# Kernel tuning notes

Measured on AMD Instinct MI355X. Metric: run time of the kernel, lower is better.

Reference implementation:

```python
import jax, jax.numpy as jnp
import numpy as np

PI = 3.141592653589793


def conv2d(x, w, b=None, padding=0, groups=1):
    out = jax.lax.conv_general_dilated(
        x, w, window_strides=(1, 1), padding=((padding, padding), (padding, padding)),
        dimension_numbers=('NCHW', 'OIHW', 'NCHW'), feature_group_count=groups)
    if b is not None:
        out = out + b.reshape(1, -1, 1, 1)
    return out


def group_norm(x, weight, bias, num_groups, eps=1e-5):
    B, C, H, W = x.shape
    xg = x.reshape(B, num_groups, C // num_groups, H, W)
    mean = xg.mean(axis=(2, 3, 4), keepdims=True)
    var = xg.var(axis=(2, 3, 4), keepdims=True)
    xg = (xg - mean) / jnp.sqrt(var + eps)
    return xg.reshape(B, C, H, W) * weight.reshape(1, -1, 1, 1) + bias.reshape(1, -1, 1, 1)


def l2norm(x, eps=1e-12):
    n = jnp.sqrt(jnp.sum(x * x, axis=1, keepdims=True))
    return x / jnp.maximum(n, eps)


def dense_sift(x):
    # kornia DenseSIFTDescriptor defaults: 8 angle bins, 4x4 spatial bins, bin size 4,
    # stride 1, padding 1, rootsift=True, clipval=0.2. Input (B,1,H,W) -> (B,128,H,W).
    eps = 1e-10
    B, C, H, W = x.shape
    # spatial_gradient(x, 'diff'), normalized: central differences / 2, replicate pad
    p = jnp.pad(x, ((0, 0), (0, 0), (1, 1), (1, 1)), mode='edge')
    gx = (p[:, :, 1:-1, 2:] - p[:, :, 1:-1, :-2]) * 0.5
    gy = (p[:, :, 2:, 1:-1] - p[:, :, :-2, 1:-1]) * 0.5
    mag = jnp.sqrt(gx * gx + gy * gy + eps)
    ori = jnp.arctan2(gy, gx + eps) + 2.0 * PI
    o_big = 8.0 * ori / (2.0 * PI)
    bo0f = jnp.floor(o_big)
    wo1 = o_big - bo0f
    bo0 = bo0f % 8
    bo1 = (bo0 + 1) % 8
    wo0m = (1.0 - wo1) * mag
    wo1m = wo1 * mag
    bins = jnp.arange(8, dtype=x.dtype).reshape(1, 8, 1, 1)
    # soft orientation-histogram binning -> (B,8,H,W)
    ang = jnp.where(bo0 == bins, wo0m, 0.0) + jnp.where(bo1 == bins, wo1m, 0.0)
    # triangular bin pooling kernel (ksize=4), depthwise conv, pad 2 -> (B,8,H+1,W+1)
    ks2 = 2.0
    xc2 = ks2 - jnp.abs(jnp.arange(4, dtype=x.dtype) + 0.5 - ks2)
    pk = jnp.outer(xc2, xc2) / (ks2 ** 2)
    pk = jnp.tile(pk.reshape(1, 1, 4, 4), (8, 1, 1, 1))
    pooled = jax.lax.conv_general_dilated(
        ang, pk, (1, 1), ((2, 2), (2, 2)),
        dimension_numbers=('NCHW', 'OIHW', 'NCHW'), feature_group_count=8)
    # PoolingConv with identity reshape kernel (k=4, pad=1) == 4x4 patch extraction
    pp = jnp.pad(pooled, ((0, 0), (0, 0), (1, 1), (1, 1)))
    patches = jnp.stack([pp[:, :, y:y + H, xx:xx + W]
                         for y in range(4) for xx in range(4)], axis=2)  # (B,8,16,H,W)
    out = patches.reshape(B, 128, H, W)
    out = jnp.clip(l2norm(out), 0.0, 0.2)
    out = l2norm(out)
    # rootsift: sqrt(L1-normalized + eps)
    l1 = jnp.sum(jnp.abs(out), axis=1, keepdims=True)
    out = jnp.sqrt(out / jnp.maximum(l1, 1e-12) + eps)
    return out


def gauss1d(ks, sigma):
    t = jnp.arange(ks, dtype=jnp.float32) - (ks - 1) / 2.0
    g = jnp.exp(-(t * t) / (2.0 * sigma * sigma))
    return g / g.sum()


def joint_bilateral_blur(inp, guidance, ks=5, sigma_color=0.1, sigma_space=(1.5, 1.5)):
    # kornia joint_bilateral_blur: border_type='reflect', color_distance_type='l1'
    B, C, H, W = inp.shape
    pad = ks // 2
    pi_ = jnp.pad(inp, ((0, 0), (0, 0), (pad, pad), (pad, pad)), mode='reflect')
    pg = jnp.pad(guidance, ((0, 0), (0, 0), (pad, pad), (pad, pad)), mode='reflect')

    def unfold(p):  # (B,C,H,W,ks*ks), flatten order (dy, dx)
        return jnp.stack([p[:, :, y:y + H, x:x + W]
                          for y in range(ks) for x in range(ks)], axis=-1)

    ui = unfold(pi_)
    ug = unfold(pg)
    diff = ug - guidance[..., None]
    cdist_sq = jnp.square(jnp.sum(jnp.abs(diff), axis=1, keepdims=True))  # L1 over channels, squared
    color_k = jnp.exp(-0.5 / (sigma_color ** 2) * cdist_sq)               # (B,1,H,W,K2)
    space_k = jnp.outer(gauss1d(ks, sigma_space[0]), gauss1d(ks, sigma_space[1])).reshape(1, 1, 1, 1, -1)
    kernel = space_k * color_k
    return (ui * kernel).sum(-1) / kernel.sum(-1)


def setup_inputs() -> dict:
    key = jax.random.key(0)
    ks = jax.random.split(key, 8)
    B, H, W = 4, 270, 512

    def wgt(k, shape, scale=0.05):
        return jax.random.normal(k, shape, dtype=jnp.float32) * scale

    z = lambda n: jnp.zeros((n,), dtype=jnp.float32)
    o = lambda n: jnp.ones((n,), dtype=jnp.float32)
    return {
        'x': jax.random.normal(ks[0], (B, 1, H, W), dtype=jnp.float32),
        'w1': wgt(ks[1], (64, 128, 5, 5)), 'b1': z(64), 'g1w': o(64), 'g1b': z(64),
        'w2': wgt(ks[2], (32, 64, 3, 3)), 'b2': z(32), 'g2w': o(32), 'g2b': z(32),
        'w3': wgt(ks[3], (16, 32, 3, 3)), 'b3': z(16), 'g3w': o(16), 'g3b': z(16),
        'w4': wgt(ks[4], (8, 16, 3, 3)), 'b4': z(8), 'g4w': o(8), 'g4b': z(8),
        'w5': wgt(ks[5], (2, 8, 3, 3)), 'b5': z(2),
        'sw1': wgt(ks[6], (32, 128, 1, 1)), 'sb1': z(32),
        'sw2': wgt(ks[7], (8, 32, 1, 1)), 'sb2': z(8),
    }


def reference(x, w1, b1, g1w, g1b, w2, b2, g2w, g2b, w3, b3, g3w, g3b,
              w4, b4, g4w, g4b, w5, b5, sw1, sb1, sw2, sb2):
    orig = x
    s = dense_sift(x)                                     # (B,128,H,W)
    h = jax.nn.relu(group_norm(conv2d(s, w1, b1, 2), g1w, g1b, 8))
    h = jax.nn.relu(group_norm(conv2d(h, w2, b2, 1), g2w, g2b, 8))
    h = h + conv2d(s, sw1, sb1, 0)                        # skip 1
    blk = h
    h = jax.nn.relu(group_norm(conv2d(h, w3, b3, 1), g3w, g3b, 4))
    h = jax.nn.relu(group_norm(conv2d(h, w4, b4, 1), g4w, g4b, 4))
    h = h + conv2d(blk, sw2, sb2, 0)                      # skip 2
    h = conv2d(h, w5, b5, 1)                              # (B,2,H,W)
    guide = jnp.tile(orig, (1, 2, 1, 1))
    h = joint_bilateral_blur(h, guide, ks=5, sigma_color=0.1, sigma_space=(1.5, 1.5))
    h = jnp.tanh(h)
    scale = jnp.array([0.436, 0.615], dtype=h.dtype).reshape(1, 2, 1, 1)
    return h * scale
```

## Files before the change

### kernel.cpp

```cpp
#include <hip/hip_runtime.h>

#define DEV __device__ __forceinline__

typedef __bf16 bf16x8 __attribute__((ext_vector_type(8)));
typedef float f32x4 __attribute__((ext_vector_type(4)));

union U8 { uint4 q; unsigned short u[8]; };

constexpr int BN = 4, H = 270, W = 512, HW = H * W;
constexpr int IH5 = 274, P5 = 516;
constexpr int IH3 = 272, P3 = 514;

DEV unsigned short f2bf(float f) {
  unsigned int u = __builtin_bit_cast(unsigned int, f);
  u = (u + 0x7FFFu + ((u >> 16) & 1u)) >> 16;
  return (unsigned short)u;
}
DEV float bf2f(unsigned short h) {
  return __builtin_bit_cast(float, (unsigned int)h << 16);
}

#define GLL16(g, l)                                                                        \
  __builtin_amdgcn_global_load_lds((const __attribute__((address_space(1))) void*)(g),     \
                                   (__attribute__((address_space(3))) void*)(l), 16, 0, 0)

DEV int swz(int row) { return ((row >> 1) & 3) << 4; }

__global__ void k_fill(float* __restrict__ out, int n, float v) {
  int i = blockIdx.x * 256 + threadIdx.x;
  if (i < n) out[i] = v;
}

template <int C, int PD>
__global__ void k_halo(unsigned short* __restrict__ buf, int IHt, int pitch, int nb_) {
  int vPerRow = pitch * C / 8;
  int topBot = 2 * PD * vPerRow;
  int sideV = PD * C / 8;
  int midRows = IHt - 2 * PD;
  int perS = topBot + midRows * 2 * sideV;
  int v = blockIdx.x * 256 + threadIdx.x;
  if (v >= nb_ * perS) return;
  int s = v / perS, r = v % perS;
  size_t base = (size_t)s * IHt * pitch * C;
  size_t off;
  if (r < topBot) {
    int half = r / (PD * vPerRow);
    int rr = r % (PD * vPerRow);
    off = ((size_t)(half ? (IHt - PD) : 0) * pitch * C) + (size_t)rr * 8;
  } else {
    int r2 = r - topBot;
    int row = r2 / (2 * sideV), c2 = r2 % (2 * sideV);
    int side = c2 / sideV, cc = c2 % sideV;
    off = ((size_t)(PD + row) * pitch + (side ? (pitch - PD) : 0)) * C + (size_t)cc * 8;
  }
  *(uint4*)(buf + base + off) = uint4{0, 0, 0, 0};
}

__global__ void k_sift_ang(const float* __restrict__ x, float* __restrict__ ang, int nTot) {
  int p = blockIdx.x * 256 + threadIdx.x;
  if (p >= nTot) return;
  int b = p / HW, r = p % HW, y = r / W, xx = r % W;
  const float* xb = x + (size_t)b * HW;
  float xm = xb[y * W + (xx > 0 ? xx - 1 : 0)];
  float xp = xb[y * W + (xx < W - 1 ? xx + 1 : W - 1)];
  float ym = xb[(y > 0 ? y - 1 : 0) * W + xx];
  float yp = xb[(y < H - 1 ? y + 1 : H - 1) * W + xx];
  float gx = (xp - xm) * 0.5f, gy = (yp - ym) * 0.5f;
  float mag = sqrtf(gx * gx + gy * gy + 1e-10f);
  float ori = atan2f(gy, gx + 1e-10f) + 6.2831855f;
  float o = (8.0f * ori) / 6.2831855f;
  float bo0f = floorf(o);
  float wo1 = o - bo0f;
  int b0 = ((int)bo0f) & 7;
  int b1 = (b0 + 1) & 7;
  float w0m = (1.0f - wo1) * mag, w1m = wo1 * mag;
  float v[8];
#pragma unroll
  for (int k = 0; k < 8; ++k)
    v[k] = (k == b0 ? w0m : 0.0f) + (k == b1 ? w1m : 0.0f);
  float4* o4 = (float4*)(ang + (size_t)p * 8);
  o4[0] = make_float4(v[0], v[1], v[2], v[3]);
  o4[1] = make_float4(v[4], v[5], v[6], v[7]);
}

__global__ void k_sift_pool(const float* __restrict__ ang, float* __restrict__ pooled, int nTot) {
  constexpr int PH = H + 1, PW = W + 1;
  int p = blockIdx.x * 256 + threadIdx.x;
  if (p >= nTot) return;
  int b = p / (PH * PW), r = p % (PH * PW), y = r / PW, xx = r % PW;
  float4 a0 = {0, 0, 0, 0}, a1 = {0, 0, 0, 0};
  const float xc2[4] = {0.5f, 1.5f, 1.5f, 0.5f};
#pragma unroll
  for (int ky = 0; ky < 4; ++ky) {
    int yy = y - 2 + ky;
    if (yy < 0 || yy >= H) continue;
#pragma unroll
    for (int kx = 0; kx < 4; ++kx) {
      int xs = xx - 2 + kx;
      if (xs < 0 || xs >= W) continue;
      float w = xc2[ky] * xc2[kx] * 0.25f;
      const float4* s4 = (const float4*)(ang + ((size_t)(b * H + yy) * W + xs) * 8);
      float4 v0 = s4[0], v1 = s4[1];
      a0.x += w * v0.x; a0.y += w * v0.y; a0.z += w * v0.z; a0.w += w * v0.w;
      a1.x += w * v1.x; a1.y += w * v1.y; a1.z += w * v1.z; a1.w += w * v1.w;
    }
  }
  float4* o4 = (float4*)(pooled + (size_t)p * 8);
  o4[0] = a0; o4[1] = a1;
}

__global__ void k_sift_desc(const float* __restrict__ pooled, unsigned short* __restrict__ spad) {
  constexpr int PH = H + 1, PW = W + 1;
  int tid = threadIdx.x;
  int wv = tid >> 6, lane = tid & 63;
  int p = blockIdx.x * 4 + wv;
  int b = p / HW, r = p % HW, yy = r / W, xx = r % W;
  int a = lane >> 3, jj = lane & 7;
  int j0 = jj * 2;
  int dy = j0 >> 2, dx = j0 & 3;
  int rr = yy + dy - 1;
  int c0 = xx + dx - 1, c1 = c0 + 1;
  bool rv = (rr >= 0 && rr <= H);
  int rc = min(max(rr, 0), H);
  const float* pb = pooled + ((size_t)(b * PH + rc) * PW) * 8 + a;
  float v0 = 0.0f, v1 = 0.0f;
  if (rv && c0 >= 0 && c0 <= W) v0 = pb[(size_t)c0 * 8];
  if (rv && c1 >= 0 && c1 <= W) v1 = pb[(size_t)c1 * 8];

  float n2 = v0 * v0 + v1 * v1;
#pragma unroll
  for (int m = 1; m < 64; m <<= 1) n2 += __shfl_xor(n2, m);
  float inv = 1.0f / fmaxf(sqrtf(n2), 1e-12f);
  v0 = fminf(v0 * inv, 0.2f);
  v1 = fminf(v1 * inv, 0.2f);
  float S = v0 + v1;
#pragma unroll
  for (int m = 1; m < 64; m <<= 1) S += __shfl_xor(S, m);
  float iS = 1.0f / fmaxf(S, 1e-12f);
  v0 = sqrtf(v0 * iS + 1e-10f);
  v1 = sqrtf(v1 * iS + 1e-10f);
  unsigned int pk = (unsigned int)f2bf(v0) | ((unsigned int)f2bf(v1) << 16);
  *(unsigned int*)(spad + ((size_t)(b * IH5 + yy + 2) * P5 + xx + 2) * 128 + lane * 2) = pk;
}

template <int CIN, int COUT, int KS>
__global__ void k_prep(const float* __restrict__ w, unsigned short* __restrict__ wbuf) {
  int i = blockIdx.x * 256 + threadIdx.x;
  if (i >= KS * KS * COUT * CIN) return;
  int t = i / (COUT * CIN), r2 = i % (COUT * CIN), co = r2 / CIN, e = r2 % CIN;
  wbuf[i] = f2bf(w[(co * CIN + e) * (KS * KS) + t]);
}

DEV int xcd_remap(int bid, int nbid) {
  int q8 = nbid >> 3, r8 = nbid & 7;
  int xcd = bid & 7;
  return (xcd < r8 ? xcd * (q8 + 1) : r8 * (q8 + 1) + (xcd - r8) * q8) + (bid >> 3);
}

template <int CIN, int COUT, int KS, int NG, int MINW, bool FSKIP, int BMPX>
__launch_bounds__(BMPX, MINW)
__global__ void k_convr(const unsigned short* __restrict__ in, int IHt, int ipitch,
                        const unsigned short* __restrict__ wtap,
                        const float* __restrict__ bias,
                        const unsigned short* __restrict__ wsk,
                        const float* __restrict__ skb,
                        unsigned short* __restrict__ outraw,
                        unsigned short* __restrict__ skraw,
                        float* __restrict__ part, int nbid) {
  constexpr int NWV = BMPX / 64;
  constexpr int NXB = 512 / BMPX;
  constexpr int SLABPX = BMPX + KS - 1;
  constexpr int KQ = CIN / 32;
  constexpr int NF = COUT / 16;
  constexpr int SLAB = SLABPX * 64;
  constexpr int SWQ = COUT * 64;
  constexpr int SWROW = KS * SWQ;
  constexpr int SSK = FSKIP ? 32 * 64 : 16;
  constexpr int STRIDE = BMPX * 16;
  __shared__ __align__(16) unsigned char slabB[2][SLAB];
  __shared__ __align__(16) unsigned char wrowB[2][SWROW];
  __shared__ __align__(16) unsigned char wskB[2][SSK];
  __shared__ float red[NWV][16];

  int tid = threadIdx.x;
  int lane = tid & 63, wid = tid >> 6;
  int l15 = lane & 15, hi = lane >> 4;

  int byl = xcd_remap(blockIdx.x, nbid);
  int half = byl % NXB, rowid = byl / NXB;
  int y = rowid % H, b = rowid / H;
  int x0 = half * BMPX;

  f32x4 acc[4][NF] = {};
  f32x4 ask[4][2] = {};

  auto stage = [&](int it, int pbuf) {
    int q = it / KS, ky = it % KS;
    const char* src = (const char*)(in + ((size_t)(b * IHt + y + ky) * ipitch + x0) * CIN + q * 32);
    for (int d = tid * 16; d < SLAB; d += STRIDE) {
      int px = d >> 6, qb = d & 63;
      GLL16(src + px * (CIN * 2) + (qb ^ swz(px)), slabB[pbuf] + d);
    }
    const char* wsrc = (const char*)wtap + (size_t)(ky * KS) * (COUT * CIN * 2) + q * 64;
    for (int d = tid * 16; d < SWROW; d += STRIDE) {
      int kx = d / SWQ, rem = d % SWQ;
      int co = rem >> 6, qb = rem & 63;
      GLL16(wsrc + (size_t)kx * (COUT * CIN * 2) + co * (CIN * 2) + (qb ^ swz(co)), wrowB[pbuf] + d);
    }
  };
  auto stage_wsk = [&](int q, int pbuf) {
    const char* src = (const char*)wsk + q * 64;
    for (int d = tid * 16; d < 32 * 64; d += STRIDE) {
      int co = d >> 6, qb = d & 63;
      GLL16(src + co * (CIN * 2) + (qb ^ swz(co)), wskB[pbuf] + d);
    }
  };

  stage(0, 0);
  if constexpr (FSKIP) stage_wsk(0, 0);
  __syncthreads();

#pragma unroll 1
  for (int it = 0; it < KQ * KS; ++it) {
    int cur = it & 1;
    int q = it / KS, ky = it % KS;
    if (it + 1 < KQ * KS) {
      stage(it + 1, cur ^ 1);
      if (FSKIP && (it + 1) % KS == 0) stage_wsk((it + 1) / KS, ((it + 1) / KS) & 1);
    }
    const unsigned char* sl = slabB[cur];
    const unsigned char* wr = wrowB[cur];
    int koff = hi * 16;
#pragma unroll
    for (int kx = 0; kx < KS; ++kx) {
      bf16x8 af[4];
#pragma unroll
      for (int mi = 0; mi < 4; ++mi) {
        int px = wid * 64 + mi * 16 + l15 + kx;
        af[mi] = *(const bf16x8*)(sl + px * 64 + (koff ^ swz(px)));
      }
#pragma unroll
      for (int ni = 0; ni < NF; ++ni) {
        int co = ni * 16 + l15;
        bf16x8 bq = *(const bf16x8*)(wr + kx * SWQ + co * 64 + (koff ^ swz(co)));
#pragma unroll
        for (int mi = 0; mi < 4; ++mi)
          acc[mi][ni] = __builtin_amdgcn_mfma_f32_16x16x32_bf16(af[mi], bq, acc[mi][ni], 0, 0, 0);
      }
      if constexpr (FSKIP) {
        if (ky == KS / 2 && kx == KS / 2) {
#pragma unroll
          for (int ni = 0; ni < 2; ++ni) {
            int co = ni * 16 + l15;
            bf16x8 bq = *(const bf16x8*)(wskB[q & 1] + co * 64 + (koff ^ swz(co)));
#pragma unroll
            for (int mi = 0; mi < 4; ++mi)
              ask[mi][ni] = __builtin_amdgcn_mfma_f32_16x16x32_bf16(af[mi], bq, ask[mi][ni], 0, 0, 0);
          }
        }
      }
    }
    __syncthreads();
  }

#pragma unroll
  for (int ni = 0; ni < NF; ++ni) {
    float bv = bias[ni * 16 + l15];
#pragma unroll
    for (int mi = 0; mi < 4; ++mi)
#pragma unroll
      for (int rr = 0; rr < 4; ++rr)
        acc[mi][ni][rr] += bv;
  }
  unsigned short* op = outraw + ((size_t)(b * H + y) * W + x0) * COUT;
#pragma unroll
  for (int mi = 0; mi < 4; ++mi)
#pragma unroll
    for (int rr = 0; rr < 4; ++rr) {
      int px = wid * 64 + mi * 16 + hi * 4 + rr;
#pragma unroll
      for (int ni = 0; ni < NF; ++ni)
        op[(size_t)px * COUT + ni * 16 + l15] = f2bf(acc[mi][ni][rr]);
    }
  if constexpr (FSKIP) {
    unsigned short* ops = skraw + ((size_t)(b * H + y) * W + x0) * 32;
#pragma unroll
    for (int ni = 0; ni < 2; ++ni) {
      float bv = skb[ni * 16 + l15];
#pragma unroll
      for (int mi = 0; mi < 4; ++mi)
#pragma unroll
        for (int rr = 0; rr < 4; ++rr)
          ask[mi][ni][rr] += bv;
    }
#pragma unroll
    for (int mi = 0; mi < 4; ++mi)
#pragma unroll
      for (int rr = 0; rr < 4; ++rr) {
        int px = wid * 64 + mi * 16 + hi * 4 + rr;
#pragma unroll
        for (int ni = 0; ni < 2; ++ni)
          ops[(size_t)px * 32 + ni * 16 + l15] = f2bf(ask[mi][ni][rr]);
      }
  }
  if constexpr (NG > 0) {
    constexpr int GPC = COUT / NG;
#pragma unroll
    for (int ni = 0; ni < NF; ++ni) {
      float s = 0.0f, q2 = 0.0f;
#pragma unroll
      for (int mi = 0; mi < 4; ++mi)
#pragma unroll
        for (int rr = 0; rr < 4; ++rr) {
          float v = acc[mi][ni][rr];
          s += v; q2 += v * v;
        }
      s += __shfl_xor(s, 16); q2 += __shfl_xor(q2, 16);
      s += __shfl_xor(s, 32); q2 += __shfl_xor(q2, 32);
#pragma unroll
      for (int m = 1; m < GPC; m <<= 1) { s += __shfl_xor(s, m); q2 += __shfl_xor(q2, m); }
      if (hi == 0 && (l15 % GPC) == 0) {
        int g = ni * (16 / GPC) + l15 / GPC;
        red[wid][g] = s;
        red[wid][NG + g] = q2;
      }
    }
    __syncthreads();
    if (tid < 2 * NG) {
      float t = 0.0f;
#pragma unroll
      for (int wv2 = 0; wv2 < NWV; ++wv2) t += red[wv2][tid];
      part[(size_t)byl * (2 * NG) + tid] = t;
    }
  }
}

template <int CIN, int COUT, int KS, int NG, bool ADDSK>
__launch_bounds__(512, 4)
__global__ void k_convf(const unsigned short* __restrict__ in,
                        const unsigned short* __restrict__ skin,
                        const unsigned short* __restrict__ wtap,
                        const float* __restrict__ bias,
                        const float* __restrict__ scg, const float* __restrict__ shg,
                        unsigned short* __restrict__ outraw,
                        float* __restrict__ part, int nbid) {
  constexpr int SLABPX = 512 + KS - 1;
  constexpr int KQ = CIN / 32;
  constexpr int NF = COUT / 16;
  constexpr int SLAB = SLABPX * 64;
  constexpr int SWQ = COUT * 64;
  constexpr int SWROW = KS * SWQ;
  __shared__ __align__(16) unsigned char slabB[2][SLAB];
  __shared__ __align__(16) unsigned char wrowB[2][SWROW];
  __shared__ float scS[CIN], shS[CIN];
  __shared__ float red[8][16];

  int tid = threadIdx.x;
  int lane = tid & 63, wid = tid >> 6;
  int l15 = lane & 15, hi = lane >> 4;

  int byl = xcd_remap(blockIdx.x, nbid);
  int y = byl % H, b = byl / H;

  if (tid < CIN) { scS[tid] = scg[b * CIN + tid]; shS[tid] = shg[b * CIN + tid]; }
  __syncthreads();

  f32x4 acc[4][NF] = {};

  auto stage = [&](int it, int pbuf) {
    int q = it / KS, ky = it % KS;
    int row = y + ky - 1;
    bool rowok = (row >= 0 && row < H);
    for (int d = tid * 16; d < SLAB; d += 8192) {
      int px = d >> 6, qb = d & 63;
      int x = px - 1;
      U8 o; o.q = uint4{0, 0, 0, 0};
      if (rowok && x >= 0 && x < W) {
        size_t e = ((size_t)(b * H + row) * W + x) * CIN + q * 32;
        U8 u; u.q = *(const uint4*)((const char*)in + e * 2 + qb);
        U8 s;
        if (ADDSK) s.q = *(const uint4*)((const char*)skin + e * 2 + qb);
        int cb = q * 32 + (qb >> 1);
#pragma unroll
        for (int j = 0; j < 8; ++j) {
          float f = fmaxf(bf2f(u.u[j]) * scS[cb + j] + shS[cb + j], 0.0f);
          if (ADDSK) f += bf2f(s.u[j]);
          o.u[j] = f2bf(f);
        }
      }
      *(uint4*)(slabB[pbuf] + px * 64 + (qb ^ swz(px))) = o.q;
    }
    const char* wsrc = (const char*)wtap + (size_t)(ky * KS) * (COUT * CIN * 2) + q * 64;
    for (int d = tid * 16; d < SWROW; d += 8192) {
      int kx = d / SWQ, rem = d % SWQ;
      int co = rem >> 6, qb = rem & 63;
      GLL16(wsrc + (size_t)kx * (COUT * CIN * 2) + co * (CIN * 2) + (qb ^ swz(co)), wrowB[pbuf] + d);
    }
  };

  stage(0, 0);
  __syncthreads();

#pragma unroll 1
  for (int it = 0; it < KQ * KS; ++it) {
    int cur = it & 1;
    if (it + 1 < KQ * KS) stage(it + 1, cur ^ 1);
    const unsigned char* sl = slabB[cur];
    const unsigned char* wr = wrowB[cur];
    int koff = hi * 16;
#pragma unroll
    for (int kx = 0; kx < KS; ++kx) {
      bf16x8 af[4];
#pragma unroll
      for (int mi = 0; mi < 4; ++mi) {
        int px = wid * 64 + mi * 16 + l15 + kx;
        af[mi] = *(const bf16x8*)(sl + px * 64 + (koff ^ swz(px)));
      }
#pragma unroll
      for (int ni = 0; ni < NF; ++ni) {
        int co = ni * 16 + l15;
        bf16x8 bq = *(const bf16x8*)(wr + kx * SWQ + co * 64 + (koff ^ swz(co)));
#pragma unroll
        for (int mi = 0; mi < 4; ++mi)
          acc[mi][ni] = __builtin_amdgcn_mfma_f32_16x16x32_bf16(af[mi], bq, acc[mi][ni], 0, 0, 0);
      }
    }
    __syncthreads();
  }

#pragma unroll
  for (int ni = 0; ni < NF; ++ni) {
    float bv = bias[ni * 16 + l15];
#pragma unroll
    for (int mi = 0; mi < 4; ++mi)
#pragma unroll
      for (int rr = 0; rr < 4; ++rr)
        acc[mi][ni][rr] += bv;
  }
  unsigned short* op = outraw + ((size_t)(b * H + y) * W) * COUT;
#pragma unroll
  for (int mi = 0; mi < 4; ++mi)
#pragma unroll
    for (int rr = 0; rr < 4; ++rr) {
      int px = wid * 64 + mi * 16 + hi * 4 + rr;
#pragma unroll
      for (int ni = 0; ni < NF; ++ni)
        op[(size_t)px * COUT + ni * 16 + l15] = f2bf(acc[mi][ni][rr]);
    }
  if constexpr (NG > 0) {
    constexpr int GPC = COUT / NG;
#pragma unroll
    for (int ni = 0; ni < NF; ++ni) {
      float s = 0.0f, q2 = 0.0f;
#pragma unroll
      for (int mi = 0; mi < 4; ++mi)
#pragma unroll
        for (int rr = 0; rr < 4; ++rr) {
          float v = acc[mi][ni][rr];
          s += v; q2 += v * v;
        }
      s += __shfl_xor(s, 16); q2 += __shfl_xor(q2, 16);
      s += __shfl_xor(s, 32); q2 += __shfl_xor(q2, 32);
#pragma unroll
      for (int m = 1; m < GPC; m <<= 1) { s += __shfl_xor(s, m); q2 += __shfl_xor(q2, m); }
      if (hi == 0 && (l15 % GPC) == 0) {
        int g = ni * (16 / GPC) + l15 / GPC;
        red[wid][g] = s;
        red[wid][NG + g] = q2;
      }
    }
    __syncthreads();
    if (tid < 2 * NG) {
      float t = 0.0f;
#pragma unroll
      for (int wv2 = 0; wv2 < 8; ++wv2) t += red[wv2][tid];
      part[(size_t)byl * (2 * NG) + tid] = t;
    }
  }
}

template <int COUT, int NG>
__global__ void k_gn_fin(const float* __restrict__ part, int NB,
                         const float* __restrict__ gw, const float* __restrict__ gb,
                         float* __restrict__ scale, float* __restrict__ shift, float invN) {
  constexpr int GPC = COUT / NG;
  int b = blockIdx.x / NG, g = blockIdx.x % NG;
  int lane = threadIdx.x;
  float s = 0.0f, q = 0.0f;
  for (int i = lane; i < NB; i += 64) {
    const float* pp = part + (size_t)(b * NB + i) * (2 * NG);
    s += pp[g]; q += pp[NG + g];
  }
#pragma unroll
  for (int m = 1; m < 64; m <<= 1) { s += __shfl_xor(s, m); q += __shfl_xor(q, m); }
  if (lane == 0) {
    float mean = s * invN;
    float var = q * invN - mean * mean;
    float rstd = rsqrtf(var + 1e-5f);
#pragma unroll
    for (int j = 0; j < GPC; ++j) {
      int c = g * GPC + j;
      float sc = gw[c] * rstd;
      scale[b * COUT + c] = sc;
      shift[b * COUT + c] = gb[c] - mean * sc;
    }
  }
}

__global__ void k_conv4(const unsigned short* __restrict__ h3raw, const float* __restrict__ w4,
                        const float* __restrict__ b4,
                        const float* __restrict__ sc3, const float* __restrict__ sh3,
                        unsigned short* __restrict__ h4raw, float* __restrict__ part) {
  __shared__ float wl[1152];
  __shared__ float scs[16], shs[16];
  __shared__ float red[4][8];
  int b0 = (blockIdx.x * 256) / HW;
  for (int i = threadIdx.x; i < 1152; i += 256) {
    int t = i / 128, r2 = i % 128, ci = r2 >> 3, co = r2 & 7;
    wl[i] = w4[(co * 16 + ci) * 9 + t];
  }
  if (threadIdx.x < 16) { scs[threadIdx.x] = sc3[b0 * 16 + threadIdx.x]; shs[threadIdx.x] = sh3[b0 * 16 + threadIdx.x]; }
  __syncthreads();
  int p = blockIdx.x * 256 + threadIdx.x;
  int b = p / HW, r = p % HW, y = r / W, xx = r % W;
  float acc[8];
#pragma unroll
  for (int co = 0; co < 8; ++co) acc[co] = b4[co];
#pragma unroll
  for (int t = 0; t < 9; ++t) {
    int ky = t / 3, kx = t % 3;
    int row = y + ky - 1, x = xx + kx - 1;
    if (row < 0 || row >= H || x < 0 || x >= W) continue;
    const unsigned short* ip = h3raw + ((size_t)(b * H + row) * W + x) * 16;
    U8 u0, u1;
    u0.q = *(const uint4*)ip;
    u1.q = *(const uint4*)(ip + 8);
#pragma unroll
    for (int ci = 0; ci < 16; ++ci) {
      float raw = bf2f(ci < 8 ? u0.u[ci] : u1.u[ci - 8]);
      float iv = fmaxf(raw * scs[ci] + shs[ci], 0.0f);
#pragma unroll
      for (int co = 0; co < 8; ++co)
        acc[co] += iv * wl[t * 128 + ci * 8 + co];
    }
  }
  int lane = threadIdx.x & 63, wv = threadIdx.x >> 6;
  float s[4], q[4];
#pragma unroll
  for (int g = 0; g < 4; ++g) {
    s[g] = acc[2 * g] + acc[2 * g + 1];
    q[g] = acc[2 * g] * acc[2 * g] + acc[2 * g + 1] * acc[2 * g + 1];
  }
#pragma unroll
  for (int m = 1; m < 64; m <<= 1) {
#pragma unroll
    for (int g = 0; g < 4; ++g) { s[g] += __shfl_xor(s[g], m); q[g] += __shfl_xor(q[g], m); }
  }
  if (lane == 0) {
#pragma unroll
    for (int g = 0; g < 4; ++g) { red[wv][g] = s[g]; red[wv][4 + g] = q[g]; }
  }
  __syncthreads();
  if (threadIdx.x < 8)
    part[(size_t)blockIdx.x * 8 + threadIdx.x] =
        red[0][threadIdx.x] + red[1][threadIdx.x] + red[2][threadIdx.x] + red[3][threadIdx.x];
  U8 o;
#pragma unroll
  for (int co = 0; co < 8; ++co) o.u[co] = f2bf(acc[co]);
  *(uint4*)(h4raw + (size_t)p * 8) = o.q;
}

__global__ void k_norm4(const unsigned short* __restrict__ h4raw,
                        const unsigned short* __restrict__ h2raw,
                        const unsigned short* __restrict__ sk1,
                        const float* __restrict__ sc2, const float* __restrict__ sh2,
                        const float* __restrict__ sc4, const float* __restrict__ sh4,
                        const float* __restrict__ sw2, const float* __restrict__ sb2,
                        unsigned short* __restrict__ blk2pad) {
  __shared__ float wl[256];
  __shared__ float s2[32], h2s[32];
  int b0 = (blockIdx.x * 256) / HW;
  {
    int i = threadIdx.x;
    int ci = i >> 3, co = i & 7;
    wl[i] = sw2[co * 32 + ci];
    if (i < 32) { s2[i] = sc2[b0 * 32 + i]; h2s[i] = sh2[b0 * 32 + i]; }
  }
  __syncthreads();
  int p = blockIdx.x * 256 + threadIdx.x;
  int b = p / HW, r = p % HW, y = r / W, xx = r % W;
  float acc[8];
#pragma unroll
  for (int co = 0; co < 8; ++co) acc[co] = sb2[co];
  const unsigned short* hp2 = h2raw + (size_t)p * 32;
  const unsigned short* skp = sk1 + (size_t)p * 32;
#pragma unroll
  for (int half = 0; half < 4; ++half) {
    U8 u; u.q = *(const uint4*)(hp2 + half * 8);
    U8 s; s.q = *(const uint4*)(skp + half * 8);
#pragma unroll
    for (int j = 0; j < 8; ++j) {
      int ci = half * 8 + j;
      float blk = fmaxf(bf2f(u.u[j]) * s2[ci] + h2s[ci], 0.0f) + bf2f(s.u[j]);
#pragma unroll
      for (int co = 0; co < 8; ++co) acc[co] += blk * wl[ci * 8 + co];
    }
  }
  U8 hv; hv.q = *(const uint4*)(h4raw + (size_t)p * 8);
  U8 o;
#pragma unroll
  for (int co = 0; co < 8; ++co) {
    float f = fmaxf(bf2f(hv.u[co]) * sc4[b * 8 + co] + sh4[b * 8 + co], 0.0f) + acc[co];
    o.u[co] = f2bf(f);
  }
  size_t cbase = ((size_t)(b * IH3 + y + 1) * P3 + (xx + 1));
  *(uint4*)(blk2pad + cbase * 8) = o.q;
}

__global__ void k_conv5(const unsigned short* __restrict__ blk2pad, const float* __restrict__ w5,
                        const float* __restrict__ b5, float* __restrict__ h5) {
  __shared__ float wl[144];
  if (threadIdx.x < 144) {
    int i = threadIdx.x;
    int t = i / 16, r2 = i % 16, ci = r2 >> 1, co = r2 & 1;
    wl[i] = w5[(co * 8 + ci) * 9 + t];
  }
  __syncthreads();
  int p = blockIdx.x * 256 + threadIdx.x;
  int b = p / HW, r = p % HW, y = r / W, xx = r % W;
  float a0 = b5[0], a1 = b5[1];
#pragma unroll
  for (int t = 0; t < 9; ++t) {
    int ky = t / 3, kx = t % 3;
    const unsigned short* ip = blk2pad + ((size_t)(b * IH3 + y + ky) * P3 + (xx + kx)) * 8;
    U8 u; u.q = *(const uint4*)ip;
#pragma unroll
    for (int ci = 0; ci < 8; ++ci) {
      float iv = bf2f(u.u[ci]);
      a0 += iv * wl[t * 16 + ci * 2];
      a1 += iv * wl[t * 16 + ci * 2 + 1];
    }
  }
  h5[(size_t)p * 2] = a0;
  h5[(size_t)p * 2 + 1] = a1;
}

__global__ void k_bilateral(const float* __restrict__ h5, const float* __restrict__ x,
                            float* __restrict__ out, int nTot) {
  int p = blockIdx.x * 256 + threadIdx.x;
  if (p >= nTot) return;
  int b = p / HW, r = p % HW, y = r / W, xx = r % W;
  const float* xb = x + (size_t)b * HW;
  float xc = xb[r];
  float e1 = expf(-1.0f / 4.5f), e0 = expf(-4.0f / 4.5f);
  float gs = 1.0f + 2.0f * e1 + 2.0f * e0;
  float g[5] = {e0 / gs, e1 / gs, 1.0f / gs, e1 / gs, e0 / gs};
  float n0 = 0.0f, n1 = 0.0f, den = 0.0f;
#pragma unroll
  for (int dy = 0; dy < 5; ++dy) {
    int yn = y + dy - 2;
    yn = yn < 0 ? -yn : (yn >= H ? 2 * H - 2 - yn : yn);
#pragma unroll
    for (int dx = 0; dx < 5; ++dx) {
      int xn = xx + dx - 2;
      xn = xn < 0 ? -xn : (xn >= W ? 2 * W - 2 - xn : xn);
      float xv = xb[yn * W + xn];
      float d = xv - xc;
      float wgt = g[dy] * g[dx] * expf(-200.0f * d * d);
      den += wgt;
      const float* hp = h5 + ((size_t)(b * HW) + yn * W + xn) * 2;
      n0 += wgt * hp[0];
      n1 += wgt * hp[1];
    }
  }
  float o0 = tanhf(n0 / den) * 0.436f;
  float o1 = tanhf(n1 / den) * 0.615f;
  out[(size_t)(b * 2) * HW + r] = o0;
  out[(size_t)(b * 2 + 1) * HW + r] = o1;
}

extern "C" void kernel_launch(void* const* d_in, const int* in_sizes, int n_in,
                              void* d_out, int out_size, void* d_ws, size_t ws_size,
                              hipStream_t stream) {
  (void)in_sizes; (void)n_in; (void)out_size;
  const float* x   = (const float*)d_in[0];
  const float* w1  = (const float*)d_in[1];
  const float* b1  = (const float*)d_in[2];
  const float* g1w = (const float*)d_in[3];
  const float* g1b = (const float*)d_in[4];
  const float* w2  = (const float*)d_in[5];
  const float* b2  = (const float*)d_in[6];
  const float* g2w = (const float*)d_in[7];
  const float* g2b = (const float*)d_in[8];
  const float* w3  = (const float*)d_in[9];
  const float* b3  = (const float*)d_in[10];
  const float* g3w = (const float*)d_in[11];
  const float* g3b = (const float*)d_in[12];
  const float* w4  = (const float*)d_in[13];
  const float* b4  = (const float*)d_in[14];
  const float* g4w = (const float*)d_in[15];
  const float* g4b = (const float*)d_in[16];
  const float* w5  = (const float*)d_in[17];
  const float* b5  = (const float*)d_in[18];
  const float* sw1 = (const float*)d_in[19];
  const float* sb1 = (const float*)d_in[20];
  const float* sw2 = (const float*)d_in[21];
  const float* sb2 = (const float*)d_in[22];
  float* out = (float*)d_out;
  char* ws = (char*)d_ws;

  auto AL = [](size_t v) { return (v + 255) & ~(size_t)255; };
  const size_t sSPAD  = (size_t)IH5 * P5 * 128 * 2;
  const size_t sANG   = (size_t)HW * 8 * 4;
  const size_t sH1RAW = (size_t)HW * 64 * 2;
  const size_t sH1PAD = (size_t)IH3 * P3 * 64 * 2;
  const size_t sH2RAW = (size_t)HW * 32 * 2;
  const size_t sH3RAW = (size_t)HW * 16 * 2;
  const size_t sH4RAW = (size_t)HW * 8 * 2;
  const size_t sBLK2  = (size_t)IH3 * P3 * 8 * 2;

  int nb = 0;
  size_t offB = 0, offSmall = 0;
  const size_t smallFixed = AL(1024 * 1024) + AL((size_t)4 * 1080 * 16 * 4) + 8 * 4096;
  for (int cand = 4; cand >= 1; cand >>= 1) {
    size_t oB   = AL((size_t)cand * sSPAD);
    size_t oH1P = AL(oB + (size_t)cand * sH1RAW);
    size_t oS   = AL(oH1P + (size_t)cand * sH1PAD);
    size_t need = oS + smallFixed + AL((size_t)cand * sH2RAW);
    if (ws_size >= need) { nb = cand; offB = oB; offSmall = oS; break; }
  }
  if (nb == 0) {
    k_fill<<<(BN * 2 * HW + 255) / 256, 256, 0, stream>>>(out, BN * 2 * HW, 123.0f);
    return;
  }

  size_t oWB1  = offSmall;
  size_t oWB2  = AL(oWB1 + 25 * 64 * 128 * 2);
  size_t oWB3  = AL(oWB2 + 9 * 32 * 64 * 2);
  size_t oWBS  = AL(oWB3 + 9 * 16 * 32 * 2);
  size_t oPART = AL(oWBS + 32 * 128 * 2);
  size_t oSC1  = AL(oPART + (size_t)4 * 1080 * 16 * 4);
  size_t oSC2  = oSC1 + 4096, oSC3 = oSC2 + 4096, oSC4 = oSC3 + 4096;
  size_t oSK1  = oSC4 + 4096;

  unsigned short* wb1  = (unsigned short*)(ws + oWB1);
  unsigned short* wb2  = (unsigned short*)(ws + oWB2);
  unsigned short* wb3  = (unsigned short*)(ws + oWB3);
  unsigned short* wbs1 = (unsigned short*)(ws + oWBS);
  float* part = (float*)(ws + oPART);
  float* sc1 = (float*)(ws + oSC1); float* sh1 = sc1 + nb * 64;
  float* sc2 = (float*)(ws + oSC2); float* sh2 = sc2 + nb * 32;
  float* sc3 = (float*)(ws + oSC3); float* sh3 = sc3 + nb * 16;
  float* sc4 = (float*)(ws + oSC4); float* sh4 = sc4 + nb * 8;
  unsigned short* sk1 = (unsigned short*)(ws + oSK1);

  k_prep<128, 64, 5><<<800, 256, 0, stream>>>(w1, wb1);
  k_prep<64, 32, 3><<<72, 256, 0, stream>>>(w2, wb2);
  k_prep<32, 16, 3><<<18, 256, 0, stream>>>(w3, wb3);
  k_prep<128, 32, 1><<<16, 256, 0, stream>>>(sw1, wbs1);

  size_t u0 = AL((size_t)nb * sH2RAW);
  size_t u1 = AL(u0 + (size_t)nb * sH3RAW);
  size_t u2 = AL(u1 + (size_t)nb * sH4RAW);
  size_t u3 = AL(u2 + (size_t)nb * sBLK2);

  for (int b0 = 0; b0 < BN; b0 += nb) {
    const float* x_c = x + (size_t)b0 * HW;
    float* out_c = out + (size_t)b0 * 2 * HW;
    unsigned short* spad   = (unsigned short*)(ws);
    float*          ang    = (float*)(ws + offB);
    float*          pooled = (float*)(ws + AL(offB + (size_t)nb * sANG));
    unsigned short* h1raw  = (unsigned short*)(ws + offB);
    unsigned short* h2raw  = (unsigned short*)(ws);
    unsigned short* h3raw  = (unsigned short*)(ws + u0);
    unsigned short* h4raw  = (unsigned short*)(ws + u1);
    unsigned short* blk2   = (unsigned short*)(ws + u2);
    float*          h5     = (float*)(ws + u3);
    int nHW = nb * HW;

    k_halo<128, 2><<<(nb * 50304 + 255) / 256, 256, 0, stream>>>(spad, IH5, P5, nb);

    k_sift_ang<<<nb * 540, 256, 0, stream>>>(x_c, ang, nHW);
    int nPP = nb * (H + 1) * (W + 1);
    k_sift_pool<<<(nPP + 255) / 256, 256, 0, stream>>>(ang, pooled, nPP);
    k_sift_desc<<<nHW / 4, 256, 0, stream>>>(pooled, spad);

    int n1 = nb * H * 2;
    k_convr<128, 64, 5, 8, 2, true, 256><<<n1, 256, 0, stream>>>(
        spad, IH5, P5, wb1, b1, wbs1, sb1, h1raw, sk1, part, n1);
    k_gn_fin<64, 8><<<nb * 8, 64, 0, stream>>>(part, 2 * H, g1w, g1b, sc1, sh1, 1.0f / (8.0f * HW));

    int n2 = nb * H;
    k_convf<64, 32, 3, 8, false><<<n2, 512, 0, stream>>>(
        h1raw, nullptr, wb2, b2, sc1, sh1, h2raw, part, n2);
    k_gn_fin<32, 8><<<nb * 8, 64, 0, stream>>>(part, H, g2w, g2b, sc2, sh2, 1.0f / (4.0f * HW));

    k_convf<32, 16, 3, 4, true><<<n2, 512, 0, stream>>>(
        h2raw, sk1, wb3, b3, sc2, sh2, h3raw, part, n2);
    k_gn_fin<16, 4><<<nb * 4, 64, 0, stream>>>(part, H, g3w, g3b, sc3, sh3, 1.0f / (4.0f * HW));

    k_conv4<<<nb * 540, 256, 0, stream>>>(h3raw, w4, b4, sc3, sh3, h4raw, part);
    k_gn_fin<8, 4><<<nb * 4, 64, 0, stream>>>(part, 540, g4w, g4b, sc4, sh4, 1.0f / (2.0f * HW));

    k_halo<8, 1><<<(nb * 1568 + 255) / 256, 256, 0, stream>>>(blk2, IH3, P3, nb);
    k_norm4<<<nb * 540, 256, 0, stream>>>(h4raw, h2raw, sk1, sc2, sh2, sc4, sh4, sw2, sb2, blk2);

    k_conv5<<<nb * 540, 256, 0, stream>>>(blk2, w5, b5, h5);
    k_bilateral<<<nb * 540, 256, 0, stream>>>(h5, x_c, out_c, nHW);
  }
}
```

Measured before the change: 673.1 us.

## Use two waves per conv1 block with larger per-wave tiles and merge prep launches

The first 5x5 conv kernel now runs with 2 waves per 256-pixel block instead of 4, so each wave owns 8 M-fragments and reuses each B-operand LDS read across twice as many MFMAs. Launch bounds drop to MINW=1, which allows many more accumulator registers per wave but may lower occupancy, and staging loops now do twice as many iterations per thread. The four weight-prep kernels are also merged into a single launch to cut launch overhead.

Measured after the change: 775.5 us. 1.15x slower.

```diff
diff --git a/kernel.cpp b/kernel.cpp
--- a/kernel.cpp
+++ b/kernel.cpp
@@ -143,13 +143,36 @@
   *(unsigned int*)(spad + ((size_t)(b * IH5 + yy + 2) * P5 + xx + 2) * 128 + lane * 2) = pk;
 }
 
-template <int CIN, int COUT, int KS>
-__global__ void k_prep(const float* __restrict__ w, unsigned short* __restrict__ wbuf) {
+__global__ void k_prep_all(const float* __restrict__ w1, const float* __restrict__ w2,
+                           const float* __restrict__ w3, const float* __restrict__ sw1,
+                           unsigned short* __restrict__ wb1, unsigned short* __restrict__ wb2,
+                           unsigned short* __restrict__ wb3, unsigned short* __restrict__ wbs1) {
+  constexpr int N1 = 25 * 64 * 128, N2 = 9 * 32 * 64, N3 = 9 * 16 * 32, N4 = 32 * 128;
   int i = blockIdx.x * 256 + threadIdx.x;
-  if (i >= KS * KS * COUT * CIN) return;
-  int t = i / (COUT * CIN), r2 = i % (COUT * CIN), co = r2 / CIN, e = r2 % CIN;
-  wbuf[i] = f2bf(w[(co * CIN + e) * (KS * KS) + t]);
-}
+  if (i < N1) {
+    int t = i / (64 * 128), r2 = i % (64 * 128), co = r2 / 128, e = r2 % 128;
+    wb1[i] = f2bf(w1[(co * 128 + e) * 25 + t]);
+    return;
+  }
+  int i2 = i - N1;
+  if (i2 < N2) {
+    int t = i2 / (32 * 64), r2 = i2 % (32 * 64), co = r2 / 64, e = r2 % 64;
+    wb2[i2] = f2bf(w2[(co * 64 + e) * 9 + t]);
+    return;
+  }
+  int i3 = i2 - N2;
+  if (i3 < N3) {
+    int t = i3 / (16 * 32), r2 = i3 % (16 * 32), co = r2 / 32, e = r2 % 32;
+    wb3[i3] = f2bf(w3[(co * 32 + e) * 9 + t]);
+    return;
+  }
+  int i4 = i3 - N3;
+  if (i4 < N4) {
+    int co = i4 / 128, e = i4 % 128;
+    wbs1[i4] = f2bf(sw1[co * 128 + e]);
+  }
+}
+constexpr int PREP_TOT = 25 * 64 * 128 + 9 * 32 * 64 + 9 * 16 * 32 + 32 * 128;
 
 DEV int xcd_remap(int bid, int nbid) {
   int q8 = nbid >> 3, r8 = nbid & 7;
@@ -157,8 +180,8 @@
   return (xcd < r8 ? xcd * (q8 + 1) : r8 * (q8 + 1) + (xcd - r8) * q8) + (bid >> 3);
 }
 
-template <int CIN, int COUT, int KS, int NG, int MINW, bool FSKIP, int BMPX>
-__launch_bounds__(BMPX, MINW)
+template <int CIN, int COUT, int KS, int NG, int MINW, bool FSKIP, int BMPX, int NWV>
+__launch_bounds__(NWV * 64, MINW)
 __global__ void k_convr(const unsigned short* __restrict__ in, int IHt, int ipitch,
                         const unsigned short* __restrict__ wtap,
                         const float* __restrict__ bias,
@@ -167,7 +190,7 @@
                         unsigned short* __restrict__ outraw,
                         unsigned short* __restrict__ skraw,
                         float* __restrict__ part, int nbid) {
-  constexpr int NWV = BMPX / 64;
+  constexpr int MI = BMPX / (16 * NWV);
   constexpr int NXB = 512 / BMPX;
   constexpr int SLABPX = BMPX + KS - 1;
   constexpr int KQ = CIN / 32;
@@ -176,7 +199,7 @@
   constexpr int SWQ = COUT * 64;
   constexpr int SWROW = KS * SWQ;
   constexpr int SSK = FSKIP ? 32 * 64 : 16;
-  constexpr int STRIDE = BMPX * 16;
+  constexpr int STRIDE = NWV * 64 * 16;
   __shared__ __align__(16) unsigned char slabB[2][SLAB];
   __shared__ __align__(16) unsigned char wrowB[2][SWROW];
   __shared__ __align__(16) unsigned char wskB[2][SSK];
@@ -191,8 +214,8 @@
   int y = rowid % H, b = rowid / H;
   int x0 = half * BMPX;
 
-  f32x4 acc[4][NF] = {};
-  f32x4 ask[4][2] = {};
+  f32x4 acc[MI][NF] = {};
+  f32x4 ask[MI][2] = {};
 
   auto stage = [&](int it, int pbuf) {
     int q = it / KS, ky = it % KS;
@@ -233,10 +256,10 @@
     int koff = hi * 16;
 #pragma unroll
     for (int kx = 0; kx < KS; ++kx) {
-      bf16x8 af[4];
-#pragma unroll
-      for (int mi = 0; mi < 4; ++mi) {
-        int px = wid * 64 + mi * 16 + l15 + kx;
+      bf16x8 af[MI];
+#pragma unroll
+      for (int mi = 0; mi < MI; ++mi) {
+        int px = wid * (MI * 16) + mi * 16 + l15 + kx;
         af[mi] = *(const bf16x8*)(sl + px * 64 + (koff ^ swz(px)));
       }
 #pragma unroll
@@ -244,7 +267,7 @@
         int co = ni * 16 + l15;
         bf16x8 bq = *(const bf16x8*)(wr + kx * SWQ + co * 64 + (koff ^ swz(co)));
 #pragma unroll
-        for (int mi = 0; mi < 4; ++mi)
+        for (int mi = 0; mi < MI; ++mi)
           acc[mi][ni] = __builtin_amdgcn_mfma_f32_16x16x32_bf16(af[mi], bq, acc[mi][ni], 0, 0, 0);
       }
       if constexpr (FSKIP) {
@@ -254,7 +277,7 @@
             int co = ni * 16 + l15;
             bf16x8 bq = *(const bf16x8*)(wskB[q & 1] + co * 64 + (koff ^ swz(co)));
 #pragma unroll
-            for (int mi = 0; mi < 4; ++mi)
+            for (int mi = 0; mi < MI; ++mi)
               ask[mi][ni] = __builtin_amdgcn_mfma_f32_16x16x32_bf16(af[mi], bq, ask[mi][ni], 0, 0, 0);
           }
         }
@@ -267,17 +290,17 @@
   for (int ni = 0; ni < NF; ++ni) {
     float bv = bias[ni * 16 + l15];
 #pragma unroll
-    for (int mi = 0; mi < 4; ++mi)
+    for (int mi = 0; mi < MI; ++mi)
 #pragma unroll
       for (int rr = 0; rr < 4; ++rr)
         acc[mi][ni][rr] += bv;
   }
   unsigned short* op = outraw + ((size_t)(b * H + y) * W + x0) * COUT;
 #pragma unroll
-  for (int mi = 0; mi < 4; ++mi)
+  for (int mi = 0; mi < MI; ++mi)
 #pragma unroll
     for (int rr = 0; rr < 4; ++rr) {
-      int px = wid * 64 + mi * 16 + hi * 4 + rr;
+      int px = wid * (MI * 16) + mi * 16 + hi * 4 + rr;
 #pragma unroll
       for (int ni = 0; ni < NF; ++ni)
         op[(size_t)px * COUT + ni * 16 + l15] = f2bf(acc[mi][ni][rr]);
@@ -288,16 +311,16 @@
     for (int ni = 0; ni < 2; ++ni) {
       float bv = skb[ni * 16 + l15];
 #pragma unroll
-      for (int mi = 0; mi < 4; ++mi)
+      for (int mi = 0; mi < MI; ++mi)
 #pragma unroll
         for (int rr = 0; rr < 4; ++rr)
           ask[mi][ni][rr] += bv;
     }
 #pragma unroll
-    for (int mi = 0; mi < 4; ++mi)
+    for (int mi = 0; mi < MI; ++mi)
 #pragma unroll
       for (int rr = 0; rr < 4; ++rr) {
-        int px = wid * 64 + mi * 16 + hi * 4 + rr;
+        int px = wid * (MI * 16) + mi * 16 + hi * 4 + rr;
 #pragma unroll
         for (int ni = 0; ni < 2; ++ni)
           ops[(size_t)px * 32 + ni * 16 + l15] = f2bf(ask[mi][ni][rr]);
@@ -309,7 +332,7 @@
     for (int ni = 0; ni < NF; ++ni) {
       float s = 0.0f, q2 = 0.0f;
 #pragma unroll
-      for (int mi = 0; mi < 4; ++mi)
+      for (int mi = 0; mi < MI; ++mi)
 #pragma unroll
         for (int rr = 0; rr < 4; ++rr) {
           float v = acc[mi][ni][rr];
@@ -754,10 +777,7 @@
   float* sc4 = (float*)(ws + oSC4); float* sh4 = sc4 + nb * 8;
   unsigned short* sk1 = (unsigned short*)(ws + oSK1);
 
-  k_prep<128, 64, 5><<<800, 256, 0, stream>>>(w1, wb1);
-  k_prep<64, 32, 3><<<72, 256, 0, stream>>>(w2, wb2);
-  k_prep<32, 16, 3><<<18, 256, 0, stream>>>(w3, wb3);
-  k_prep<128, 32, 1><<<16, 256, 0, stream>>>(sw1, wbs1);
+  k_prep_all<<<(PREP_TOT + 255) / 256, 256, 0, stream>>>(w1, w2, w3, sw1, wb1, wb2, wb3, wbs1);
 
   size_t u0 = AL((size_t)nb * sH2RAW);
   size_t u1 = AL(u0 + (size_t)nb * sH3RAW);
@@ -786,7 +806,7 @@
     k_sift_desc<<<nHW / 4, 256, 0, stream>>>(pooled, spad);
 
     int n1 = nb * H * 2;
-    k_convr<128, 64, 5, 8, 2, true, 256><<<n1, 256, 0, stream>>>(
+    k_convr<128, 64, 5, 8, 1, true, 256, 2><<<n1, 128, 0, stream>>>(
         spad, IH5, P5, wb1, b1, wbs1, sb1, h1raw, sk1, part, n1);
     k_gn_fin<64, 8><<<nb * 8, 64, 0, stream>>>(part, 2 * H, g1w, g1b, sc1, sh1, 1.0f / (8.0f * HW));
 
```
